# Kernel tuning notes

Measured on AMD Instinct MI355X. Metric: run time of the kernel, lower is better.

The kernel has to match this reference:

```python
import jax, jax.numpy as jnp
import numpy as np

B, N, O, C, D = 1, 256, 12, 128, 32  # batch, points, orientations, num_hidden, basis_dim


def setup_inputs() -> dict:
    key = jax.random.key(0)
    k0, k1, k2, k3, k4, k5 = jax.random.split(key, 6)
    return {
        "x": jax.random.normal(k0, (B, N, O, C), dtype=jnp.float32),
        "kernel_basis": jax.random.normal(k1, (B, N, N, O, D), dtype=jnp.float32),
        "fiber_kernel_basis": jax.random.normal(k2, (O, O, D), dtype=jnp.float32),
        "mask": jnp.ones((B, N), dtype=jnp.float32),
        "W_spatial": jax.random.normal(k3, (D, C), dtype=jnp.float32) / np.sqrt(D),
        "W_rot": jax.random.normal(k4, (D, C), dtype=jnp.float32) / np.sqrt(D),
        "bias": jnp.zeros((C,), dtype=jnp.float32),
    }


def reference(x, kernel_basis, fiber_kernel_basis, mask, W_spatial, W_rot, bias):
    # Dense (no bias) projections of the bases: last dim D -> C
    spatial_kernel = jnp.einsum("bmnod,dc->bmnoc", kernel_basis, W_spatial)  # (B,M,N,O,C)
    rot_kernel = jnp.einsum("pod,dc->poc", fiber_kernel_basis, W_rot)        # (O,O,C)
    # spatial aggregation over source points n (mask-weighted)
    y = jnp.einsum("bnoc,bmnoc,bn->bmoc", x, spatial_kernel, mask)           # (B,M,O,C)
    # fiber (orientation) rotation, averaged over o
    y = jnp.einsum("bmoc,poc->bmpc", y, rot_kernel) / rot_kernel.shape[-2]   # (B,M,O,C)
    return y + bias
```

## Files before the change

kernel.cpp:

```cpp
#include <hip/hip_runtime.h>
#include <hip/hip_bf16.h>

#define N_ 256
#define M_ 256
#define O_ 12
#define C_ 128
#define D_ 32
#define S2 16
#define KBROW 393216

typedef __attribute__((ext_vector_type(8))) short short8;
typedef __attribute__((ext_vector_type(4))) float floatx4;

#define GLD16(GSRC, LDST) \
    __builtin_amdgcn_global_load_lds( \
        (const __attribute__((address_space(1))) void*)(GSRC), \
        (__attribute__((address_space(3))) void*)(LDST), 16, 0, 0)

static __device__ __forceinline__ short2 pk2(float a, float b) {
    union { __hip_bfloat162 h; short2 s; } u;
    u.h = __float22bfloat162_rn(make_float2(a, b));
    return u.s;
}

static __device__ __forceinline__ short f2bf(float f) {
    unsigned u = __float_as_uint(f);
    unsigned r = u + 0x7FFFu + ((u >> 16) & 1u);
    return (short)(r >> 16);
}

static __device__ __forceinline__ float bf2f(short s) {
    return __uint_as_float(((unsigned)(unsigned short)s) << 16);
}

__global__ __launch_bounds__(256) void prep2_kernel(
    const float* __restrict__ x, const float* __restrict__ mask,
    const float* __restrict__ fkb, const float* __restrict__ Wr,
    float* __restrict__ xmm, float* __restrict__ rk)
{
    const int b = blockIdx.x;
    const int t = threadIdx.x;
    if (b < 1536) {
        const int idx = b * 256 + t;
        const int n = idx / (O_ * C_);
        xmm[idx] = x[idx] * mask[n];
    } else {
        const int idx = (b - 1536) * 256 + t;
        const int c  = idx & (C_ - 1);
        const int po = idx >> 7;
        const float* f = fkb + po * D_;
        float acc = 0.f;
#pragma unroll
        for (int d = 0; d < D_; ++d) acc = fmaf(f[d], Wr[d * C_ + c], acc);
        rk[idx] = acc;
    }
}

__global__ __launch_bounds__(768, 3) void spatial8_kernel(
    const float* __restrict__ kb, const float* __restrict__ xmm,
    const float* __restrict__ Ws, short* __restrict__ part16)
{
    const int mt  = blockIdx.x;
    const int sck = blockIdx.y;
    const int t = threadIdx.x;
    const int lane = t & 63;
    const int w = t >> 6;
    const int l15 = lane & 15;
    const int lk  = lane >> 4;
    const int m0 = mt * 16;
    const int n0 = sck * 16;

    __shared__ __align__(16) char Abuf[2 * 49152];

    const char* kbc = (const char*)kb;
#define MKSRC(CI) (kbc + (size_t)(m0 + (CI) / 192) * KBROW \
                       + (size_t)n0 * 1536 \
                       + (size_t)((((CI) % 192) ^ (((CI) / 192) & 7)) * 16))
    const char* s0_ = MKSRC(t);
    const char* s1_ = MKSRC(t + 768);
    const char* s2_ = MKSRC(t + 1536);
    const char* s3_ = MKSRC(t + 2304);
#undef MKSRC
#define STAGE(BIX, S) { \
    char* db_ = Abuf + (BIX) * 49152 + w * 1024; \
    GLD16(s0_ + (size_t)(S) * 3072, db_); \
    GLD16(s1_ + (size_t)(S) * 3072, db_ + 12288); \
    GLD16(s2_ + (size_t)(S) * 3072, db_ + 24576); \
    GLD16(s3_ + (size_t)(S) * 3072, db_ + 36864); }

    short8 wsb[8];
#pragma unroll
    for (int cg = 0; cg < 8; ++cg) {
        short8 v;
#pragma unroll
        for (int i = 0; i < 8; ++i)
            v[i] = f2bf(Ws[(lk * 8 + i) * C_ + cg * 16 + l15]);
        wsb[cg] = v;
    }

    const int swz = l15 & 7;
    const int oA0 = l15 * 3072 + w * 128 + (((lk * 2)     ^ swz) * 16);
    const int oA1 = l15 * 3072 + w * 128 + (((lk * 2 + 1) ^ swz) * 16);

    const float* xb = xmm + ((size_t)n0 * O_ + w) * C_ + l15;

    floatx4 acc[8];
#pragma unroll
    for (int cg = 0; cg < 8; ++cg)
#pragma unroll
        for (int q = 0; q < 4; ++q) acc[cg][q] = 0.f;
    const floatx4 zc = {0.f, 0.f, 0.f, 0.f};

    STAGE(0, 0);

    float xvA[16], xvB[16];
#pragma unroll
    for (int k2 = 0; k2 < 2; ++k2)
#pragma unroll
        for (int cg = 0; cg < 8; ++cg)
            xvA[k2 * 8 + cg] = xb[(size_t)k2 * (O_ * C_) + cg * 16];

#define PHASE(S, XC, XN) { \
    asm volatile("s_waitcnt vmcnt(0) lgkmcnt(0)" ::: "memory"); \
    __builtin_amdgcn_s_barrier(); \
    if ((S) + 1 < 8) { \
        STAGE(((S) + 1) & 1, (S) + 1); \
        _Pragma("unroll") \
        for (int k2 = 0; k2 < 2; ++k2) \
            _Pragma("unroll") \
            for (int cg = 0; cg < 8; ++cg) \
                XN[k2 * 8 + cg] = \
                    xb[(size_t)(2 * ((S) + 1) + k2) * (O_ * C_) + cg * 16]; \
    } \
    const char* ab_ = Abuf + ((S) & 1) * 49152; \
    _Pragma("unroll") \
    for (int ksub = 0; ksub < 2; ++ksub) { \
        const floatx4 a0_ = *(const floatx4*)(ab_ + oA0 + ksub * 1536); \
        const floatx4 a1_ = *(const floatx4*)(ab_ + oA1 + ksub * 1536); \
        union { short8 v; short2 p2[4]; } au_; \
        au_.p2[0] = pk2(a0_[0], a0_[1]); au_.p2[1] = pk2(a0_[2], a0_[3]); \
        au_.p2[2] = pk2(a1_[0], a1_[1]); au_.p2[3] = pk2(a1_[2], a1_[3]); \
        _Pragma("unroll") \
        for (int cg = 0; cg < 8; ++cg) { \
            const floatx4 t_ = __builtin_amdgcn_mfma_f32_16x16x32_bf16( \
                au_.v, wsb[cg], zc, 0, 0, 0); \
            const float xc_ = XC[ksub * 8 + cg]; \
            _Pragma("unroll") \
            for (int q = 0; q < 4; ++q) \
                acc[cg][q] = fmaf(xc_, t_[q], acc[cg][q]); \
        } \
    } }

    PHASE(0, xvA, xvB)
    PHASE(1, xvB, xvA)
    PHASE(2, xvA, xvB)
    PHASE(3, xvB, xvA)
    PHASE(4, xvA, xvB)
    PHASE(5, xvB, xvA)
    PHASE(6, xvA, xvB)
    PHASE(7, xvB, xvA)
#undef PHASE
#undef STAGE

#pragma unroll
    for (int cg = 0; cg < 8; ++cg) {
        const int c = cg * 16 + l15;
#pragma unroll
        for (int j = 0; j < 4; ++j) {
            const int m = m0 + lk * 4 + j;
            part16[(((size_t)m * S2 + sck) * O_ + w) * C_ + c] = f2bf(acc[cg][j]);
        }
    }
}

__global__ __launch_bounds__(256) void fiber4_kernel(
    const short* __restrict__ part16, const float* __restrict__ rkv,
    const float* __restrict__ bias, float* __restrict__ out)
{
    const int m = blockIdx.x;
    const int t = threadIdx.x;
    __shared__ float y1L[O_][C_];

    if (t < 192) {
        const int o  = t >> 4;
        const int c0 = (t & 15) * 8;
        float a[8];
#pragma unroll
        for (int i = 0; i < 8; ++i) a[i] = 0.f;
#pragma unroll
        for (int s = 0; s < S2; ++s) {
            const short8 v = *reinterpret_cast<const short8*>(
                part16 + (((size_t)m * S2 + s) * O_ + o) * C_ + c0);
#pragma unroll
            for (int i = 0; i < 8; ++i) a[i] += bf2f(v[i]);
        }
#pragma unroll
        for (int i = 0; i < 8; ++i) y1L[o][c0 + i] = a[i];
    }
    __syncthreads();

#pragma unroll
    for (int k = t; k < O_ * C_; k += 256) {
        const int p = k >> 7;
        const int c = k & (C_ - 1);
        float a = 0.f;
#pragma unroll
        for (int o = 0; o < O_; ++o)
            a = fmaf(y1L[o][c], rkv[(p * O_ + o) * C_ + c], a);
        out[((size_t)m * O_ + p) * C_ + c] = a * (1.f / 12.f) + bias[c];
    }
}

__global__ __launch_bounds__(256) void spatial_old_kernel(
    const float* __restrict__ x, const float* __restrict__ kb,
    const float* __restrict__ mask, const float* __restrict__ Ws,
    float* __restrict__ y1)
{
    const int bid = blockIdx.x;
    const int m = bid / O_, o = bid % O_;
    const int tid = threadIdx.x;
    const int h = tid >> 7, c = tid & (C_ - 1);
    __shared__ float kbs[2][8][D_];
    __shared__ float msk[N_];
    __shared__ float Ts[2][D_][C_];
    msk[tid] = mask[tid];
    float T[D_];
#pragma unroll
    for (int d = 0; d < D_; ++d) T[d] = 0.f;
    const float* kb_mo = kb + (size_t)m * (N_ * O_ * D_) + o * D_;
    const int j_ld = c >> 4, d_ld = (c & 15) * 2;
    for (int chunk = 0; chunk < 16; ++chunk) {
        const int n0 = h * 128 + chunk * 8;
        __syncthreads();
        float2 v = *reinterpret_cast<const float2*>(
            kb_mo + (size_t)(n0 + j_ld) * (O_ * D_) + d_ld);
        kbs[h][j_ld][d_ld] = v.x;
        kbs[h][j_ld][d_ld + 1] = v.y;
        __syncthreads();
#pragma unroll
        for (int j = 0; j < 8; ++j) {
            const int n = n0 + j;
            const float xv = x[(n * O_ + o) * C_ + c] * msk[n];
#pragma unroll
            for (int d = 0; d < D_; ++d) T[d] = fmaf(kbs[h][j][d], xv, T[d]);
        }
    }
#pragma unroll
    for (int d = 0; d < D_; ++d) Ts[h][d][c] = T[d];
    __syncthreads();
    if (h == 0) {
        float a = 0.f;
#pragma unroll
        for (int d = 0; d < D_; ++d)
            a = fmaf(Ts[0][d][c] + Ts[1][d][c], Ws[d * C_ + c], a);
        y1[((size_t)m * O_ + o) * C_ + c] = a;
    }
}

__global__ __launch_bounds__(256) void fiber_old_kernel(
    const float* __restrict__ y1, const float* __restrict__ rkv,
    const float* __restrict__ bias, float* __restrict__ out)
{
    int idx = blockIdx.x * 256 + threadIdx.x;
    if (idx >= M_ * O_ * C_) return;
    int c = idx & (C_ - 1);
    int p = (idx >> 7) % O_;
    int m = idx / (O_ * C_);
    float a = 0.f;
#pragma unroll
    for (int o = 0; o < O_; ++o)
        a = fmaf(y1[(m * O_ + o) * C_ + c], rkv[(p * O_ + o) * C_ + c], a);
    out[idx] = a * (1.0f / 12.0f) + bias[c];
}

__global__ __launch_bounds__(256) void rot_proj_kernel(
    const float* __restrict__ fkb, const float* __restrict__ Wr,
    float* __restrict__ rk)
{
    int idx = blockIdx.x * 256 + threadIdx.x;
    if (idx >= O_ * O_ * C_) return;
    int c  = idx & (C_ - 1);
    int po = idx >> 7;
    const float* f = fkb + po * D_;
    float acc = 0.f;
#pragma unroll
    for (int d = 0; d < D_; ++d) acc = fmaf(f[d], Wr[d * C_ + c], acc);
    rk[idx] = acc;
}

extern "C" void kernel_launch(void* const* d_in, const int* in_sizes, int n_in,
                              void* d_out, int out_size, void* d_ws, size_t ws_size,
                              hipStream_t stream)
{
    const float* x    = (const float*)d_in[0];
    const float* kb   = (const float*)d_in[1];
    const float* fkb  = (const float*)d_in[2];
    const float* mask = (const float*)d_in[3];
    const float* Wsp  = (const float*)d_in[4];
    const float* Wrt  = (const float*)d_in[5];
    const float* bias = (const float*)d_in[6];
    float* out = (float*)d_out;

    const size_t RK_F    = (size_t)O_ * O_ * C_;
    const size_t PART_E  = (size_t)M_ * S2 * O_ * C_;
    const size_t XMM_F   = (size_t)N_ * O_ * C_;
    const size_t need    = RK_F * 4 + PART_E * 2 + XMM_F * 4;

    float* rk = (float*)d_ws;

    if (ws_size >= need) {
        short* part16 = (short*)(rk + RK_F);
        float* xmm    = (float*)(part16 + PART_E);
        prep2_kernel<<<1536 + (O_ * O_ * C_) / 256, 256, 0, stream>>>(
            x, mask, fkb, Wrt, xmm, rk);
        spatial8_kernel<<<dim3(16, 16), 768, 0, stream>>>(kb, xmm, Wsp, part16);
        fiber4_kernel<<<M_, 256, 0, stream>>>(part16, rk, bias, out);
    } else {
        float* y1 = rk + RK_F;
        rot_proj_kernel<<<(O_ * O_ * C_ + 255) / 256, 256, 0, stream>>>(fkb, Wrt, rk);
        spatial_old_kernel<<<M_ * O_, 256, 0, stream>>>(x, kb, mask, Wsp, y1);
        fiber_old_kernel<<<(M_ * O_ * C_ + 255) / 256, 256, 0, stream>>>(y1, rk, bias, out);
    }
}
```

Baseline: 38.03 us.

## Split spatial reduction over more n-chunks and stage Ws in LDS

Doubles the number of split-K chunks over source points (S2 16→32), halving each block's n range and its LDS staging buffer, and launching twice as many blocks to fill more CUs. The bf16 W_spatial fragments move from per-thread registers into a padded shared-memory table that is read inside the MFMA loop, which lowers register pressure. The x values are now loaded per phase instead of being prefetched a phase ahead. In exchange, the partial-sum buffer doubles, so fiber4 has more partials to reduce, and each phase adds LDS reads for W.

Measured after the change: 39.25 us. 1.03x slower.

```diff
diff --git a/kernel.cpp b/kernel.cpp
--- a/kernel.cpp
+++ b/kernel.cpp
@@ -6,7 +6,7 @@
 #define O_ 12
 #define C_ 128
 #define D_ 32
-#define S2 16
+#define S2 32
 #define KBROW 393216
 
 typedef __attribute__((ext_vector_type(8))) short short8;
@@ -56,7 +56,7 @@
     }
 }
 
-__global__ __launch_bounds__(768, 3) void spatial8_kernel(
+__global__ __launch_bounds__(768, 3) void spatial10_kernel(
     const float* __restrict__ kb, const float* __restrict__ xmm,
     const float* __restrict__ Ws, short* __restrict__ part16)
 {
@@ -68,39 +68,36 @@
     const int l15 = lane & 15;
     const int lk  = lane >> 4;
     const int m0 = mt * 16;
-    const int n0 = sck * 16;
-
-    __shared__ __align__(16) char Abuf[2 * 49152];
+    const int n0 = sck * 8;
+
+    __shared__ __align__(16) char Abuf[2 * 24576];
+    __shared__ __align__(16) char WsL[128 * 80];
+
+    if (t < 512) {
+        const int c  = t >> 2;
+        const int dq = (t & 3) * 8;
+        short8 v;
+#pragma unroll
+        for (int i = 0; i < 8; ++i) v[i] = f2bf(Ws[(dq + i) * C_ + c]);
+        *reinterpret_cast<short8*>(WsL + c * 80 + dq * 2) = v;
+    }
 
     const char* kbc = (const char*)kb;
-#define MKSRC(CI) (kbc + (size_t)(m0 + (CI) / 192) * KBROW \
+#define MKSRC(CI) (kbc + (size_t)(m0 + (CI) / 96) * KBROW \
                        + (size_t)n0 * 1536 \
-                       + (size_t)((((CI) % 192) ^ (((CI) / 192) & 7)) * 16))
+                       + (size_t)((((CI) % 96) ^ (((CI) / 96) & 7)) * 16))
     const char* s0_ = MKSRC(t);
     const char* s1_ = MKSRC(t + 768);
-    const char* s2_ = MKSRC(t + 1536);
-    const char* s3_ = MKSRC(t + 2304);
 #undef MKSRC
 #define STAGE(BIX, S) { \
-    char* db_ = Abuf + (BIX) * 49152 + w * 1024; \
-    GLD16(s0_ + (size_t)(S) * 3072, db_); \
-    GLD16(s1_ + (size_t)(S) * 3072, db_ + 12288); \
-    GLD16(s2_ + (size_t)(S) * 3072, db_ + 24576); \
-    GLD16(s3_ + (size_t)(S) * 3072, db_ + 36864); }
-
-    short8 wsb[8];
-#pragma unroll
-    for (int cg = 0; cg < 8; ++cg) {
-        short8 v;
-#pragma unroll
-        for (int i = 0; i < 8; ++i)
-            v[i] = f2bf(Ws[(lk * 8 + i) * C_ + cg * 16 + l15]);
-        wsb[cg] = v;
-    }
+    char* db_ = Abuf + (BIX) * 24576 + w * 1024; \
+    GLD16(s0_ + (size_t)(S) * 1536, db_); \
+    GLD16(s1_ + (size_t)(S) * 1536, db_ + 12288); }
 
     const int swz = l15 & 7;
-    const int oA0 = l15 * 3072 + w * 128 + (((lk * 2)     ^ swz) * 16);
-    const int oA1 = l15 * 3072 + w * 128 + (((lk * 2 + 1) ^ swz) * 16);
+    const int oA0 = l15 * 1536 + (((w * 8 + lk * 2)     ^ swz) * 16);
+    const int oA1 = l15 * 1536 + (((w * 8 + lk * 2 + 1) ^ swz) * 16);
+    const int oW  = l15 * 80 + lk * 16;
 
     const float* xb = xmm + ((size_t)n0 * O_ + w) * C_ + l15;
 
@@ -113,52 +110,38 @@
 
     STAGE(0, 0);
 
-    float xvA[16], xvB[16];
-#pragma unroll
-    for (int k2 = 0; k2 < 2; ++k2)
-#pragma unroll
-        for (int cg = 0; cg < 8; ++cg)
-            xvA[k2 * 8 + cg] = xb[(size_t)k2 * (O_ * C_) + cg * 16];
-
-#define PHASE(S, XC, XN) { \
+#define PHASE(S) { \
     asm volatile("s_waitcnt vmcnt(0) lgkmcnt(0)" ::: "memory"); \
     __builtin_amdgcn_s_barrier(); \
-    if ((S) + 1 < 8) { \
-        STAGE(((S) + 1) & 1, (S) + 1); \
+    if ((S) + 1 < 8) STAGE(((S) + 1) & 1, (S) + 1); \
+    float xv_[8]; \
+    _Pragma("unroll") \
+    for (int cg = 0; cg < 8; ++cg) \
+        xv_[cg] = xb[(size_t)(S) * (O_ * C_) + cg * 16]; \
+    const char* ab_ = Abuf + ((S) & 1) * 24576; \
+    const floatx4 a0_ = *(const floatx4*)(ab_ + oA0); \
+    const floatx4 a1_ = *(const floatx4*)(ab_ + oA1); \
+    union { short8 v; short2 p2[4]; } au_; \
+    au_.p2[0] = pk2(a0_[0], a0_[1]); au_.p2[1] = pk2(a0_[2], a0_[3]); \
+    au_.p2[2] = pk2(a1_[0], a1_[1]); au_.p2[3] = pk2(a1_[2], a1_[3]); \
+    _Pragma("unroll") \
+    for (int cg = 0; cg < 8; ++cg) { \
+        const short8 wsb_ = *(const short8*)(WsL + cg * 1280 + oW); \
+        const floatx4 t_ = __builtin_amdgcn_mfma_f32_16x16x32_bf16( \
+            au_.v, wsb_, zc, 0, 0, 0); \
         _Pragma("unroll") \
-        for (int k2 = 0; k2 < 2; ++k2) \
-            _Pragma("unroll") \
-            for (int cg = 0; cg < 8; ++cg) \
-                XN[k2 * 8 + cg] = \
-                    xb[(size_t)(2 * ((S) + 1) + k2) * (O_ * C_) + cg * 16]; \
-    } \
-    const char* ab_ = Abuf + ((S) & 1) * 49152; \
-    _Pragma("unroll") \
-    for (int ksub = 0; ksub < 2; ++ksub) { \
-        const floatx4 a0_ = *(const floatx4*)(ab_ + oA0 + ksub * 1536); \
-        const floatx4 a1_ = *(const floatx4*)(ab_ + oA1 + ksub * 1536); \
-        union { short8 v; short2 p2[4]; } au_; \
-        au_.p2[0] = pk2(a0_[0], a0_[1]); au_.p2[1] = pk2(a0_[2], a0_[3]); \
-        au_.p2[2] = pk2(a1_[0], a1_[1]); au_.p2[3] = pk2(a1_[2], a1_[3]); \
-        _Pragma("unroll") \
-        for (int cg = 0; cg < 8; ++cg) { \
-            const floatx4 t_ = __builtin_amdgcn_mfma_f32_16x16x32_bf16( \
-                au_.v, wsb[cg], zc, 0, 0, 0); \
-            const float xc_ = XC[ksub * 8 + cg]; \
-            _Pragma("unroll") \
-            for (int q = 0; q < 4; ++q) \
-                acc[cg][q] = fmaf(xc_, t_[q], acc[cg][q]); \
-        } \
+        for (int q = 0; q < 4; ++q) \
+            acc[cg][q] = fmaf(xv_[cg], t_[q], acc[cg][q]); \
     } }
 
-    PHASE(0, xvA, xvB)
-    PHASE(1, xvB, xvA)
-    PHASE(2, xvA, xvB)
-    PHASE(3, xvB, xvA)
-    PHASE(4, xvA, xvB)
-    PHASE(5, xvB, xvA)
-    PHASE(6, xvA, xvB)
-    PHASE(7, xvB, xvA)
+    PHASE(0)
+    PHASE(1)
+    PHASE(2)
+    PHASE(3)
+    PHASE(4)
+    PHASE(5)
+    PHASE(6)
+    PHASE(7)
 #undef PHASE
 #undef STAGE
 
@@ -313,7 +296,7 @@
         float* xmm    = (float*)(part16 + PART_E);
         prep2_kernel<<<1536 + (O_ * O_ * C_) / 256, 256, 0, stream>>>(
             x, mask, fkb, Wrt, xmm, rk);
-        spatial8_kernel<<<dim3(16, 16), 768, 0, stream>>>(kb, xmm, Wsp, part16);
+        spatial10_kernel<<<dim3(16, 32), 768, 0, stream>>>(kb, xmm, Wsp, part16);
         fiber4_kernel<<<M_, 256, 0, stream>>>(part16, rk, bias, out);
     } else {
         float* y1 = rk + RK_F;
```
